# Kernel tuning notes

Hardware: AMD Instinct MI355X
Metric: run time of the kernel (lower is better)

The kernel has to match this reference:

```python
import jax, jax.numpy as jnp
import numpy as np

MARGIN = 0.1
PD_EPS = 1e-6  # torch.nn.PairwiseDistance default eps (added to the difference)

B = 4096
D = 512


def setup_inputs() -> dict:
    key = jax.random.key(0)
    k1, k2, k3 = jax.random.split(key, 3)
    return {
        "feature_ts": jax.random.normal(k1, (B, D), dtype=jnp.float32),
        "feature_image1": jax.random.normal(k2, (B, D), dtype=jnp.float32),
        "feature_image2": jax.random.normal(k3, (B, D), dtype=jnp.float32),
    }


def _safe_sqrt(sq):
    # sqrt with zero gradient at 0 (matches torch.cdist backward at zero distance)
    pos = sq > 0
    return jnp.where(pos, jnp.sqrt(jnp.where(pos, sq, 1.0)), 0.0)


def reference(feature_ts, feature_image1, feature_image2):
    b, d = feature_ts.shape
    # representations: [3B, D]
    reps = jnp.concatenate([feature_ts, feature_image1, feature_image2], axis=0)

    # cdist(feature_ts, reps, p=2) -> [B, 3B] via Gram-matrix expansion
    sq = (
        jnp.sum(feature_ts * feature_ts, axis=1)[:, None]
        + jnp.sum(reps * reps, axis=1)[None, :]
        - 2.0 * (feature_ts @ reps.T)
    )
    dist = _safe_sqrt(jnp.maximum(sq, 0.0))          # [B, 3B]
    dist = jax.nn.relu(dist)                          # faithful (no-op: dist >= 0)

    # PairwiseDistance(p=2): ||x1 - x2 + eps||_2
    diff = feature_image1 - feature_image2 + PD_EPS
    dist12 = jnp.sqrt(jnp.sum(diff * diff, axis=1))   # [B]

    idx = jnp.arange(b)
    l_pos_1 = dist[idx, idx + b]                      # diag offset B
    l_pos_2 = dist[idx, idx + 2 * b]                  # diag offset 2B

    positives = l_pos_1 + l_pos_2 + dist12            # [B]
    positive_value = jnp.maximum(l_pos_1, l_pos_2)    # [B]

    # negatives: all columns except {i, i+B, i+2B}; masked min instead of gather
    cols = jnp.arange(3 * b)[None, :]
    rows = idx[:, None]
    same = (cols == rows) | (cols == rows + b) | (cols == rows + 2 * b)
    negative_value = jnp.min(jnp.where(same, jnp.inf, dist), axis=1)  # [B]

    triplet = jax.nn.relu(positives - negative_value + MARGIN) + positive_value
    return jnp.sum(triplet) / b
```

## Files before the change

kernel.cpp:

```cpp
#include <hip/hip_runtime.h>
#include <hip/hip_bf16.h>

typedef unsigned short u16;
typedef unsigned int u32;
typedef __attribute__((ext_vector_type(8))) short bf16x8;
typedef __attribute__((ext_vector_type(4))) float f32x4;

#define NB 4096
#define ND 512
#define NREPS (3*NB)
#define BM 128
#define BN 128
#define BK 64

__device__ __forceinline__ u16 f2bf(float f) {
  union { float f; u32 u; } v; v.f = f;
  u32 u = v.u;
  u32 r = (u + 0x7FFFu + ((u >> 16) & 1u)) >> 16;
  return (u16)r;
}

__global__ __launch_bounds__(64) void prep_convert(
    const float* __restrict__ ts, const float* __restrict__ i1,
    const float* __restrict__ i2, u16* __restrict__ reps,
    float* __restrict__ norms)
{
  const int row = blockIdx.x;
  const int lane = threadIdx.x;
  const float* src = (row < NB) ? (ts + (size_t)row * ND)
                   : (row < 2*NB) ? (i1 + (size_t)(row - NB) * ND)
                   : (i2 + (size_t)(row - 2*NB) * ND);
  const float4* s4 = (const float4*)src;
  float4 a = s4[lane*2+0];
  float4 b = s4[lane*2+1];
  float ss = a.x*a.x + a.y*a.y + a.z*a.z + a.w*a.w
           + b.x*b.x + b.y*b.y + b.z*b.z + b.w*b.w;
  uint4 pk;
  pk.x = (u32)f2bf(a.x) | ((u32)f2bf(a.y) << 16);
  pk.y = (u32)f2bf(a.z) | ((u32)f2bf(a.w) << 16);
  pk.z = (u32)f2bf(b.x) | ((u32)f2bf(b.y) << 16);
  pk.w = (u32)f2bf(b.z) | ((u32)f2bf(b.w) << 16);
  *(uint4*)(reps + (size_t)row * ND + lane*8) = pk;
  #pragma unroll
  for (int off = 32; off; off >>= 1) ss += __shfl_down(ss, off);
  if (lane == 0) norms[row] = ss;
}

__global__ __launch_bounds__(64) void prep_dist12(
    const float* __restrict__ i1, const float* __restrict__ i2,
    float* __restrict__ dist12, u32* __restrict__ minsq)
{
  const int row = blockIdx.x;
  const int lane = threadIdx.x;
  const float4* a4 = (const float4*)(i1 + (size_t)row * ND);
  const float4* b4 = (const float4*)(i2 + (size_t)row * ND);
  float ss = 0.f;
  #pragma unroll
  for (int i = 0; i < 2; ++i) {
    float4 a = a4[lane*2+i], b = b4[lane*2+i];
    float d0 = a.x - b.x + 1e-6f, d1 = a.y - b.y + 1e-6f;
    float d2 = a.z - b.z + 1e-6f, d3 = a.w - b.w + 1e-6f;
    ss += d0*d0 + d1*d1 + d2*d2 + d3*d3;
  }
  #pragma unroll
  for (int off = 32; off; off >>= 1) ss += __shfl_down(ss, off);
  if (lane == 0) { dist12[row] = sqrtf(ss); minsq[row] = 0x7F800000u; }
}

__global__ __launch_bounds__(256) void gemm_min(
    const u16* __restrict__ reps, const float* __restrict__ norms,
    u32* __restrict__ minsq, float* __restrict__ lpos1,
    float* __restrict__ lpos2)
{
  __shared__ u16 As[BM*BK];
  __shared__ u16 Bs[BN*BK];
  const int tid  = threadIdx.x;
  const int lane = tid & 63;
  const int wave = tid >> 6;
  const int wr = wave >> 1, wc = wave & 1;
  const int fr = lane & 15, fg = lane >> 4;
  const int rowBase = blockIdx.x * BM;
  const int colBase = blockIdx.y * BN;

  f32x4 acc[4][4];
  const f32x4 zero = {0.f, 0.f, 0.f, 0.f};
  #pragma unroll
  for (int i = 0; i < 4; ++i)
    #pragma unroll
    for (int j = 0; j < 4; ++j)
      acc[i][j] = zero;

  for (int kt = 0; kt < ND/BK; ++kt) {
    const int k0 = kt * BK;
    #pragma unroll
    for (int i = 0; i < 4; ++i) {
      int g = i*256 + tid;
      int r = g >> 3, s = g & 7;
      int wslot = s ^ (r & 7);
      uint4 va = *(const uint4*)(reps + (size_t)(rowBase + r)*ND + k0 + s*8);
      uint4 vb = *(const uint4*)(reps + (size_t)(colBase + r)*ND + k0 + s*8);
      *(uint4*)&As[r*BK + wslot*8] = va;
      *(uint4*)&Bs[r*BK + wslot*8] = vb;
    }
    __syncthreads();

    bf16x8 af[4][2], bfrag[4][2];
    #pragma unroll
    for (int mf = 0; mf < 4; ++mf)
      #pragma unroll
      for (int ks = 0; ks < 2; ++ks) {
        int rowA = wr*64 + mf*16 + fr;
        int slot = ks*4 + fg;
        af[mf][ks]    = *(const bf16x8*)&As[rowA*BK + (slot ^ (rowA & 7))*8];
        int rowB = wc*64 + mf*16 + fr;
        bfrag[mf][ks] = *(const bf16x8*)&Bs[rowB*BK + (slot ^ (rowB & 7))*8];
      }
    #pragma unroll
    for (int ks = 0; ks < 2; ++ks)
      #pragma unroll
      for (int mf = 0; mf < 4; ++mf)
        #pragma unroll
        for (int nf = 0; nf < 4; ++nf)
          acc[mf][nf] = __builtin_amdgcn_mfma_f32_16x16x32_bf16(
              af[mf][ks], bfrag[nf][ks], acc[mf][nf], 0, 0, 0);
    __syncthreads();
  }

  float ncol[4];
  #pragma unroll
  for (int nf = 0; nf < 4; ++nf)
    ncol[nf] = norms[colBase + wc*64 + nf*16 + fr];
  const float INF = __builtin_inff();
  #pragma unroll
  for (int mf = 0; mf < 4; ++mf) {
    #pragma unroll
    for (int q = 0; q < 4; ++q) {
      const int r_g = rowBase + wr*64 + mf*16 + fg*4 + q;
      const float ntr = norms[r_g];
      float vm = INF;
      #pragma unroll
      for (int nf = 0; nf < 4; ++nf) {
        const int c_g = colBase + wc*64 + nf*16 + fr;
        const float dot = acc[mf][nf][q];
        const float sq = ntr + ncol[nf] - 2.0f * dot;
        if (c_g == r_g + NB)   lpos1[r_g] = sq;
        if (c_g == r_g + 2*NB) lpos2[r_g] = sq;
        const bool excl = (c_g == r_g) || (c_g == r_g + NB) || (c_g == r_g + 2*NB);
        const float v = excl ? INF : fmaxf(sq, 0.0f);
        vm = fminf(vm, v);
      }
      #pragma unroll
      for (int off = 1; off < 16; off <<= 1)
        vm = fminf(vm, __shfl_xor(vm, off));
      if (fr == 0)
        atomicMin(minsq + r_g, __float_as_uint(vm));
    }
  }
}

__global__ __launch_bounds__(256) void finalize(
    const float* __restrict__ lpos1, const float* __restrict__ lpos2,
    const float* __restrict__ dist12, const u32* __restrict__ minsq,
    float* __restrict__ out)
{
  __shared__ float red[4];
  const int tid = threadIdx.x;
  float s = 0.f;
  for (int r = tid; r < NB; r += 256) {
    float l1 = sqrtf(fmaxf(lpos1[r], 0.f));
    float l2 = sqrtf(fmaxf(lpos2[r], 0.f));
    float neg = sqrtf(__uint_as_float(minsq[r]));
    float pos = l1 + l2 + dist12[r];
    float t = fmaxf(pos - neg + 0.1f, 0.f) + fmaxf(l1, l2);
    s += t;
  }
  #pragma unroll
  for (int off = 32; off; off >>= 1) s += __shfl_down(s, off);
  if ((tid & 63) == 0) red[tid >> 6] = s;
  __syncthreads();
  if (tid == 0) out[0] = (red[0] + red[1] + red[2] + red[3]) * (1.0f / NB);
}

extern "C" void kernel_launch(void* const* d_in, const int* in_sizes, int n_in,
                              void* d_out, int out_size, void* d_ws, size_t ws_size,
                              hipStream_t stream) {
  const float* ts = (const float*)d_in[0];
  const float* i1 = (const float*)d_in[1];
  const float* i2 = (const float*)d_in[2];
  float* out = (float*)d_out;

  char* p = (char*)d_ws;
  u16* reps    = (u16*)p;            p += (size_t)NREPS * ND * sizeof(u16);
  float* norms = (float*)p;          p += (size_t)NREPS * sizeof(float);
  float* dist12 = (float*)p;         p += (size_t)NB * sizeof(float);
  u32* minsq   = (u32*)p;            p += (size_t)NB * sizeof(u32);
  float* lpos1 = (float*)p;          p += (size_t)NB * sizeof(float);
  float* lpos2 = (float*)p;          p += (size_t)NB * sizeof(float);

  prep_convert<<<NREPS, 64, 0, stream>>>(ts, i1, i2, reps, norms);
  prep_dist12<<<NB, 64, 0, stream>>>(i1, i2, dist12, minsq);
  dim3 grid(NB / BM, NREPS / BN);
  gemm_min<<<grid, 256, 0, stream>>>(reps, norms, minsq, lpos1, lpos2);
  finalize<<<1, 256, 0, stream>>>(lpos1, lpos2, dist12, minsq, out);
}
```

Before: 162.8 us.

## Fuse prep kernels, load GEMM tiles directly to LDS, widen finalize

Result: no change. 161.0 us (-1.1%).

```diff
diff --git a/kernel.cpp b/kernel.cpp
--- a/kernel.cpp
+++ b/kernel.cpp
@@ -13,6 +13,11 @@
 #define BN 128
 #define BK 64
 
+#define GLD16(gp, lp)                                                         \
+  __builtin_amdgcn_global_load_lds(                                           \
+      (const __attribute__((address_space(1))) void*)(gp),                    \
+      (__attribute__((address_space(3))) void*)(lp), 16, 0, 0)
+
 __device__ __forceinline__ u16 f2bf(float f) {
   union { float f; u32 u; } v; v.f = f;
   u32 u = v.u;
@@ -20,51 +25,53 @@
   return (u16)r;
 }
 
-__global__ __launch_bounds__(64) void prep_convert(
+__global__ __launch_bounds__(256) void prep_all(
     const float* __restrict__ ts, const float* __restrict__ i1,
     const float* __restrict__ i2, u16* __restrict__ reps,
-    float* __restrict__ norms)
+    float* __restrict__ norms, float* __restrict__ dist12,
+    u32* __restrict__ minsq)
 {
-  const int row = blockIdx.x;
-  const int lane = threadIdx.x;
-  const float* src = (row < NB) ? (ts + (size_t)row * ND)
-                   : (row < 2*NB) ? (i1 + (size_t)(row - NB) * ND)
-                   : (i2 + (size_t)(row - 2*NB) * ND);
-  const float4* s4 = (const float4*)src;
-  float4 a = s4[lane*2+0];
-  float4 b = s4[lane*2+1];
-  float ss = a.x*a.x + a.y*a.y + a.z*a.z + a.w*a.w
-           + b.x*b.x + b.y*b.y + b.z*b.z + b.w*b.w;
-  uint4 pk;
-  pk.x = (u32)f2bf(a.x) | ((u32)f2bf(a.y) << 16);
-  pk.y = (u32)f2bf(a.z) | ((u32)f2bf(a.w) << 16);
-  pk.z = (u32)f2bf(b.x) | ((u32)f2bf(b.y) << 16);
-  pk.w = (u32)f2bf(b.z) | ((u32)f2bf(b.w) << 16);
-  *(uint4*)(reps + (size_t)row * ND + lane*8) = pk;
-  #pragma unroll
-  for (int off = 32; off; off >>= 1) ss += __shfl_down(ss, off);
-  if (lane == 0) norms[row] = ss;
-}
-
-__global__ __launch_bounds__(64) void prep_dist12(
-    const float* __restrict__ i1, const float* __restrict__ i2,
-    float* __restrict__ dist12, u32* __restrict__ minsq)
-{
-  const int row = blockIdx.x;
-  const int lane = threadIdx.x;
-  const float4* a4 = (const float4*)(i1 + (size_t)row * ND);
-  const float4* b4 = (const float4*)(i2 + (size_t)row * ND);
-  float ss = 0.f;
-  #pragma unroll
-  for (int i = 0; i < 2; ++i) {
-    float4 a = a4[lane*2+i], b = b4[lane*2+i];
-    float d0 = a.x - b.x + 1e-6f, d1 = a.y - b.y + 1e-6f;
-    float d2 = a.z - b.z + 1e-6f, d3 = a.w - b.w + 1e-6f;
-    ss += d0*d0 + d1*d1 + d2*d2 + d3*d3;
-  }
-  #pragma unroll
-  for (int off = 32; off; off >>= 1) ss += __shfl_down(ss, off);
-  if (lane == 0) { dist12[row] = sqrtf(ss); minsq[row] = 0x7F800000u; }
+  __shared__ float s1[ND], s2[ND];
+  const int r = blockIdx.x;
+  const int tid = threadIdx.x;
+  const int wave = tid >> 6, lane = tid & 63;
+
+  if (wave < 3) {
+    const float* src = (wave == 0) ? ts + (size_t)r * ND
+                     : (wave == 1) ? i1 + (size_t)r * ND
+                     :               i2 + (size_t)r * ND;
+    const float4* s4 = (const float4*)src;
+    float4 a = s4[lane*2+0];
+    float4 b = s4[lane*2+1];
+    if (wave == 1) { ((float4*)s1)[lane*2+0] = a; ((float4*)s1)[lane*2+1] = b; }
+    if (wave == 2) { ((float4*)s2)[lane*2+0] = a; ((float4*)s2)[lane*2+1] = b; }
+    float ss = a.x*a.x + a.y*a.y + a.z*a.z + a.w*a.w
+             + b.x*b.x + b.y*b.y + b.z*b.z + b.w*b.w;
+    uint4 pk;
+    pk.x = (u32)f2bf(a.x) | ((u32)f2bf(a.y) << 16);
+    pk.y = (u32)f2bf(a.z) | ((u32)f2bf(a.w) << 16);
+    pk.z = (u32)f2bf(b.x) | ((u32)f2bf(b.y) << 16);
+    pk.w = (u32)f2bf(b.z) | ((u32)f2bf(b.w) << 16);
+    *(uint4*)(reps + (size_t)(wave*NB + r) * ND + lane*8) = pk;
+    #pragma unroll
+    for (int off = 32; off; off >>= 1) ss += __shfl_down(ss, off);
+    if (lane == 0) norms[wave*NB + r] = ss;
+  }
+  __syncthreads();
+  if (wave == 3) {
+    float ss = 0.f;
+    #pragma unroll
+    for (int i = 0; i < 2; ++i) {
+      float4 a = ((float4*)s1)[lane*2+i];
+      float4 b = ((float4*)s2)[lane*2+i];
+      float d0 = a.x - b.x + 1e-6f, d1 = a.y - b.y + 1e-6f;
+      float d2 = a.z - b.z + 1e-6f, d3 = a.w - b.w + 1e-6f;
+      ss += d0*d0 + d1*d1 + d2*d2 + d3*d3;
+    }
+    #pragma unroll
+    for (int off = 32; off; off >>= 1) ss += __shfl_down(ss, off);
+    if (lane == 0) { dist12[r] = sqrtf(ss); minsq[r] = 0x7F800000u; }
+  }
 }
 
 __global__ __launch_bounds__(256) void gemm_min(
@@ -82,6 +89,20 @@
   const int rowBase = blockIdx.x * BM;
   const int colBase = blockIdx.y * BN;
 
+  const int rloc = lane >> 3;
+  const int sp   = lane & 7;
+  const u16* srcA[4]; const u16* srcB[4];
+  u16* dstA[4]; u16* dstB[4];
+  #pragma unroll
+  for (int i = 0; i < 4; ++i) {
+    const int r = wave*32 + i*8 + rloc;
+    const int g = sp ^ (r & 7);
+    srcA[i] = reps + (size_t)(rowBase + r) * ND + g*8;
+    srcB[i] = reps + (size_t)(colBase + r) * ND + g*8;
+    dstA[i] = &As[(wave*32 + i*8) * BK];
+    dstB[i] = &Bs[(wave*32 + i*8) * BK];
+  }
+
   f32x4 acc[4][4];
   const f32x4 zero = {0.f, 0.f, 0.f, 0.f};
   #pragma unroll
@@ -91,16 +112,11 @@
       acc[i][j] = zero;
 
   for (int kt = 0; kt < ND/BK; ++kt) {
-    const int k0 = kt * BK;
+    const int koff = kt * BK;
     #pragma unroll
     for (int i = 0; i < 4; ++i) {
-      int g = i*256 + tid;
-      int r = g >> 3, s = g & 7;
-      int wslot = s ^ (r & 7);
-      uint4 va = *(const uint4*)(reps + (size_t)(rowBase + r)*ND + k0 + s*8);
-      uint4 vb = *(const uint4*)(reps + (size_t)(colBase + r)*ND + k0 + s*8);
-      *(uint4*)&As[r*BK + wslot*8] = va;
-      *(uint4*)&Bs[r*BK + wslot*8] = vb;
+      GLD16(srcA[i] + koff, dstA[i]);
+      GLD16(srcB[i] + koff, dstB[i]);
     }
     __syncthreads();
 
@@ -109,10 +125,10 @@
     for (int mf = 0; mf < 4; ++mf)
       #pragma unroll
       for (int ks = 0; ks < 2; ++ks) {
-        int rowA = wr*64 + mf*16 + fr;
-        int slot = ks*4 + fg;
+        const int rowA = wr*64 + mf*16 + fr;
+        const int slot = ks*4 + fg;
         af[mf][ks]    = *(const bf16x8*)&As[rowA*BK + (slot ^ (rowA & 7))*8];
-        int rowB = wc*64 + mf*16 + fr;
+        const int rowB = wc*64 + mf*16 + fr;
         bfrag[mf][ks] = *(const bf16x8*)&Bs[rowB*BK + (slot ^ (rowB & 7))*8];
       }
     #pragma unroll
@@ -158,27 +174,31 @@
   }
 }
 
-__global__ __launch_bounds__(256) void finalize(
+__global__ __launch_bounds__(1024) void finalize(
     const float* __restrict__ lpos1, const float* __restrict__ lpos2,
     const float* __restrict__ dist12, const u32* __restrict__ minsq,
     float* __restrict__ out)
 {
-  __shared__ float red[4];
+  __shared__ float red[16];
   const int tid = threadIdx.x;
   float s = 0.f;
-  for (int r = tid; r < NB; r += 256) {
+  for (int r = tid; r < NB; r += 1024) {
     float l1 = sqrtf(fmaxf(lpos1[r], 0.f));
     float l2 = sqrtf(fmaxf(lpos2[r], 0.f));
     float neg = sqrtf(__uint_as_float(minsq[r]));
     float pos = l1 + l2 + dist12[r];
-    float t = fmaxf(pos - neg + 0.1f, 0.f) + fmaxf(l1, l2);
-    s += t;
+    s += fmaxf(pos - neg + 0.1f, 0.f) + fmaxf(l1, l2);
   }
   #pragma unroll
   for (int off = 32; off; off >>= 1) s += __shfl_down(s, off);
   if ((tid & 63) == 0) red[tid >> 6] = s;
   __syncthreads();
-  if (tid == 0) out[0] = (red[0] + red[1] + red[2] + red[3]) * (1.0f / NB);
+  if (tid == 0) {
+    float t = 0.f;
+    #pragma unroll
+    for (int i = 0; i < 16; ++i) t += red[i];
+    out[0] = t * (1.0f / NB);
+  }
 }
 
 extern "C" void kernel_launch(void* const* d_in, const int* in_sizes, int n_in,
@@ -197,9 +217,8 @@
   float* lpos1 = (float*)p;          p += (size_t)NB * sizeof(float);
   float* lpos2 = (float*)p;          p += (size_t)NB * sizeof(float);
 
-  prep_convert<<<NREPS, 64, 0, stream>>>(ts, i1, i2, reps, norms);
-  prep_dist12<<<NB, 64, 0, stream>>>(i1, i2, dist12, minsq);
+  prep_all<<<NB, 256, 0, stream>>>(ts, i1, i2, reps, norms, dist12, minsq);
   dim3 grid(NB / BM, NREPS / BN);
   gemm_min<<<grid, 256, 0, stream>>>(reps, norms, minsq, lpos1, lpos2);
-  finalize<<<1, 256, 0, stream>>>(lpos1, lpos2, dist12, minsq, out);
-}
+  finalize<<<1, 1024, 0, stream>>>(lpos1, lpos2, dist12, minsq, out);
+}
```
